# Performance work log

Measured on AMD Instinct MI355X. Metric: run time of the kernel, lower is better.

Reference implementation:

```python
import jax, jax.numpy as jnp
import numpy as np

F, OUT = 256, 16
H = [128, 128, 64]
B = 8192


def _normed(v, g):
    # weight_norm (torch default dim=0): w[o,:] = g[o] * v[o,:] / ||v[o,:]||
    # v: [F, out, in], g: [F, out]
    return g[..., None] * v / jnp.linalg.norm(v, axis=-1, keepdims=True)


def setup_inputs() -> dict:
    key = jax.random.key(0)
    ks = jax.random.split(key, 12)
    s = 0.1
    return {
        "tabular": jax.random.normal(ks[0], (B, 2, F), dtype=jnp.float32),
        # input layer: Linear(1, H[0]) per feature, stacked over F
        "v_in": jax.random.normal(ks[1], (F, H[0], 1), dtype=jnp.float32) * s,
        "g_in": jnp.ones((F, H[0]), dtype=jnp.float32),
        "b_in": jax.random.normal(ks[2], (F, H[0]), dtype=jnp.float32) * s,
        # dense_0: Linear(H[0], H[1])
        "v_h0": jax.random.normal(ks[3], (F, H[1], H[0]), dtype=jnp.float32) * s,
        "g_h0": jnp.ones((F, H[1]), dtype=jnp.float32),
        "b_h0": jax.random.normal(ks[4], (F, H[1]), dtype=jnp.float32) * s,
        # dense_1: Linear(H[1], H[2])
        "v_h1": jax.random.normal(ks[5], (F, H[2], H[1]), dtype=jnp.float32) * s,
        "g_h1": jnp.ones((F, H[2]), dtype=jnp.float32),
        "b_h1": jax.random.normal(ks[6], (F, H[2]), dtype=jnp.float32) * s,
        # dense_out: Linear(H[2], OUT, bias=False)
        "v_out": jax.random.normal(ks[7], (F, OUT, H[2]), dtype=jnp.float32) * s,
        "g_out": jnp.ones((F, OUT), dtype=jnp.float32),
        "bias": jnp.zeros((1, OUT), dtype=jnp.float32),
    }


def reference(tabular, v_in, g_in, b_in, v_h0, g_h0, b_h0, v_h1, g_h1, b_h1,
              v_out, g_out, bias):
    values, is_missing = tabular[:, 0, :], tabular[:, 1, :]  # [B, F]
    x = values * (1.0 - is_missing)
    # input layer: in-dim is 1, so it's an outer product with the weight column
    w0 = _normed(v_in, g_in)[:, :, 0]                       # [F, H0]
    h = jax.nn.relu(x[:, :, None] * w0[None] + b_in[None])  # [B, F, H0]
    # hidden layers (dropout is identity in eval mode)
    h = jax.nn.relu(jnp.einsum("bfi,foi->bfo", h, _normed(v_h0, g_h0)) + b_h0[None])
    h = jax.nn.relu(jnp.einsum("bfi,foi->bfo", h, _normed(v_h1, g_h1)) + b_h1[None])
    outputs = jnp.einsum("bfi,foi->bfo", h, _normed(v_out, g_out))  # [B, F, OUT]
    # feature_dropout is identity in eval mode
    logits = jnp.sum(outputs, axis=1) + bias                # [B, OUT]
    return logits, outputs
```

## Files before the change

### kernel.cpp

```cpp
#include <hip/hip_runtime.h>

typedef unsigned short u16;
typedef unsigned int   u32;
typedef __attribute__((ext_vector_type(8))) short bf16x8;
typedef __attribute__((ext_vector_type(4))) float f32x4;
typedef __attribute__((ext_vector_type(2))) float f32x2;

#define NFEAT  256
#define NBATCH 8192
#define BT     128
#define NBT    (NBATCH / BT)
#define ITERS  8

__device__ __forceinline__ u16 f2bf(float f) {
    u32 u = __builtin_bit_cast(u32, f);
    return (u16)((u + 0x7FFFu + ((u >> 16) & 1u)) >> 16);
}
__device__ __forceinline__ u32 cvtpk(float a, float b) {
    u32 r;
    asm("v_cvt_pk_bf16_f32 %0, %1, %2" : "=v"(r) : "v"(a), "v"(b));
    return r;
}
__device__ __forceinline__ f32x4 mfma16(bf16x8 a, bf16x8 b, f32x4 c) {
    return __builtin_amdgcn_mfma_f32_16x16x32_bf16(a, b, c, 0, 0, 0);
}
__device__ __forceinline__ bf16x8 frag_word0(u32 word0) {
    union { bf16x8 v; u32 w[4]; } u;
    u.w[0] = word0; u.w[1] = 0; u.w[2] = 0; u.w[3] = 0;
    return u.v;
}
__device__ __forceinline__ char* swz(char* base, int b, int col2) {
    return base + b * 256 + (col2 ^ ((b & 15) << 4));
}
__device__ __forceinline__ const char* swz(const char* base, int b, int col2) {
    return base + b * 256 + (col2 ^ ((b & 15) << 4));
}
__device__ __forceinline__ uint2 relu_pk4(f32x4 v, f32x4 bs) {
    f32x4 s = v + bs;
    return make_uint2(cvtpk(fmaxf(s[0], 0.f), fmaxf(s[1], 0.f)),
                      cvtpk(fmaxf(s[2], 0.f), fmaxf(s[3], 0.f)));
}
__device__ __forceinline__ void barrier_lgkm() {
    asm volatile("s_waitcnt lgkmcnt(0)" ::: "memory");
    __builtin_amdgcn_s_barrier();
    asm volatile("" ::: "memory");
}

__global__ void prep_w0(const float* __restrict__ v_in, const float* __restrict__ g_in,
                        u16* __restrict__ w0) {
    int i = blockIdx.x * blockDim.x + threadIdx.x;
    float v = v_in[i];
    float g = g_in[i];
    w0[i] = f2bf(v >= 0.f ? g : -g);
}

__global__ void prep_norm(const float* __restrict__ v_h0, const float* __restrict__ g_h0,
                          const float* __restrict__ v_h1, const float* __restrict__ g_h1,
                          const float* __restrict__ v_out, const float* __restrict__ g_out,
                          u16* __restrict__ w1, u16* __restrict__ w2, u16* __restrict__ w3) {
    const int wave = (blockIdx.x * blockDim.x + threadIdx.x) >> 6;
    const int lane = threadIdx.x & 63;
    if (wave < 32768 + 16384) {
        const float* src; u16* dst; float g;
        if (wave < 32768) {
            src = v_h0 + (size_t)wave * 128; dst = w1 + (size_t)wave * 128; g = g_h0[wave];
        } else {
            int r = wave - 32768;
            src = v_h1 + (size_t)r * 128; dst = w2 + (size_t)r * 128; g = g_h1[r];
        }
        f32x2 v = *(const f32x2*)(src + lane * 2);
        float ss = v[0] * v[0] + v[1] * v[1];
        #pragma unroll
        for (int off = 32; off; off >>= 1) ss += __shfl_xor(ss, off);
        float s = g * rsqrtf(ss);
        *(u32*)(dst + lane * 2) = cvtpk(v[0] * s, v[1] * s);
    } else {
        int r = wave - 49152;
        const float* src = v_out + (size_t)r * 64;
        float v = src[lane];
        float ss = v * v;
        #pragma unroll
        for (int off = 32; off; off >>= 1) ss += __shfl_xor(ss, off);
        float s = g_out[r] * rsqrtf(ss);
        w3[(size_t)r * 64 + lane] = f2bf(v * s);
    }
}

__global__ void prep_x(const float* __restrict__ tab, u16* __restrict__ x_t) {
    __shared__ u16 tile[64][65];
    const int bb = (blockIdx.x % (NBATCH / 64)) * 64;
    const int ff = (blockIdx.x / (NBATCH / 64)) * 64;
    const int tr = threadIdx.x >> 6;
    const int tc = threadIdx.x & 63;
    #pragma unroll
    for (int i = 0; i < 16; i++) {
        int b = bb + tr + i * 4;
        float val  = tab[(size_t)b * 512 + ff + tc];
        float miss = tab[(size_t)b * 512 + 256 + ff + tc];
        tile[tr + i * 4][tc] = f2bf(val * (1.f - miss));
    }
    __syncthreads();
    #pragma unroll
    for (int i = 0; i < 16; i++) {
        int fr = tr + i * 4;
        x_t[(size_t)(ff + fr) * NBATCH + bb + tc] = tile[tc][fr];
    }
}

__global__ void reduce_logits(const float* __restrict__ outputs,
                              const float* __restrict__ bias,
                              float* __restrict__ logits) {
    const int b = blockIdx.x * 4 + (threadIdx.x >> 6);
    const int lane = threadIdx.x & 63;
    const int j4 = lane & 3;
    const int fo = lane >> 2;
    const float* base = outputs + (size_t)b * (NFEAT * 16);
    f32x4 acc = {};
    #pragma unroll
    for (int it = 0; it < 16; it++) {
        f32x4 v = *(const f32x4*)(base + (fo + it * 16) * 16 + j4 * 4);
        acc[0] += v[0]; acc[1] += v[1]; acc[2] += v[2]; acc[3] += v[3];
    }
    #pragma unroll
    for (int off = 4; off < 64; off <<= 1) {
        acc[0] += __shfl_xor(acc[0], off);
        acc[1] += __shfl_xor(acc[1], off);
        acc[2] += __shfl_xor(acc[2], off);
        acc[3] += __shfl_xor(acc[3], off);
    }
    if (lane < 4) {
        f32x4 bs = *(const f32x4*)(bias + lane * 4);
        acc[0] += bs[0]; acc[1] += bs[1]; acc[2] += bs[2]; acc[3] += bs[3];
        *(f32x4*)(logits + b * 16 + lane * 4) = acc;
    }
}

__global__ __launch_bounds__(256, 2) void nam_main(
    const u16* __restrict__ x_t, const u16* __restrict__ w0g,
    const u16* __restrict__ w1g, const u16* __restrict__ w2g, const u16* __restrict__ w3g,
    const float* __restrict__ b_in, const float* __restrict__ b_h0, const float* __restrict__ b_h1,
    float* __restrict__ outputs)
{
    __shared__ u16 hA[BT * 128];
    __shared__ u16 hB[BT * 128];

    const int bid   = blockIdx.x;
    const int f     = (bid & 7) * 32 + ((bid >> 3) & 31);
    const int chunk = bid >> 8;
    const int t  = threadIdx.x;
    const int w  = t >> 6;
    const int wo = w >> 1;
    const int wb = w & 1;
    const int lane = t & 63;
    const int lo = lane & 15;
    const int hi = lane >> 4;

    bf16x8 a0f[4];
    #pragma unroll
    for (int m = 0; m < 4; m++) {
        const int o = f * 128 + wo * 64 + m * 16 + lo;
        float bi = b_in[o];
        u32 pk = (u32)w0g[o] | (cvtpk(bi, bi) << 16);
        a0f[m] = frag_word0(hi == 0 ? pk : 0u);
    }
    bf16x8 w1f[4][4];
    {
        const u16* base = w1g + ((size_t)(f * 128 + wo * 64 + lo)) * 128 + hi * 8;
        #pragma unroll
        for (int m = 0; m < 4; m++)
            #pragma unroll
            for (int ks = 0; ks < 4; ks++)
                w1f[m][ks] = *(const bf16x8*)(base + m * 2048 + ks * 32);
    }
    bf16x8 w2f[2][4];
    {
        const u16* base = w2g + ((size_t)(f * 64 + wo * 32 + lo)) * 128 + hi * 8;
        #pragma unroll
        for (int m = 0; m < 2; m++)
            #pragma unroll
            for (int ks = 0; ks < 4; ks++)
                w2f[m][ks] = *(const bf16x8*)(base + m * 2048 + ks * 32);
    }
    bf16x8 w3f[2];
    {
        const u16* base = w3g + ((size_t)(f * 16 + lo)) * 64 + hi * 8;
        #pragma unroll
        for (int ks = 0; ks < 2; ks++)
            w3f[ks] = *(const bf16x8*)(base + ks * 32);
    }
    f32x4 bs1[4];
    #pragma unroll
    for (int m = 0; m < 4; m++)
        bs1[m] = *(const f32x4*)(b_h0 + f * 128 + wo * 64 + m * 16 + hi * 4);
    f32x4 bs2[2];
    #pragma unroll
    for (int m = 0; m < 2; m++)
        bs2[m] = *(const f32x4*)(b_h1 + f * 64 + wo * 32 + m * 16 + hi * 4);

    const u16* xbase = x_t + (size_t)f * NBATCH;

    u32 xw[4];
    {
        const int bt0 = chunk * ITERS;
        #pragma unroll
        for (int n = 0; n < 4; n++)
            xw[n] = (u32)xbase[bt0 * BT + wb * 64 + n * 16 + lo];
    }

    for (int it = 0; it < ITERS; it++) {
        const int bt = chunk * ITERS + it;

        barrier_lgkm();

        {
            bf16x8 bm[4];
            #pragma unroll
            for (int n = 0; n < 4; n++)
                bm[n] = frag_word0(hi == 0 ? (xw[n] | 0x3F800000u) : 0u);
            #pragma unroll
            for (int m = 0; m < 4; m++) {
                #pragma unroll
                for (int n = 0; n < 4; n++) {
                    f32x4 d = mfma16(a0f[m], bm[n], f32x4{});
                    const int b = wb * 64 + n * 16 + lo;
                    const int col2 = (wo * 64 + m * 16 + hi * 4) * 2;
                    *(uint2*)swz((char*)hA, b, col2) =
                        make_uint2(cvtpk(fmaxf(0.f, d[0]), fmaxf(0.f, d[1])),
                                   cvtpk(fmaxf(0.f, d[2]), fmaxf(0.f, d[3])));
                }
            }
        }
        barrier_lgkm();

        {
            if (it + 1 < ITERS) {
                #pragma unroll
                for (int n = 0; n < 4; n++)
                    xw[n] = (u32)xbase[(bt + 1) * BT + wb * 64 + n * 16 + lo];
            }
            f32x4 acc[4][4] = {};
            #pragma unroll
            for (int ks = 0; ks < 4; ks++) {
                bf16x8 bm[4];
                #pragma unroll
                for (int n = 0; n < 4; n++) {
                    const int b = wb * 64 + n * 16 + lo;
                    bm[n] = *(const bf16x8*)swz((const char*)hA, b, ks * 64 + hi * 16);
                }
                __builtin_amdgcn_s_setprio(1);
                #pragma unroll
                for (int m = 0; m < 4; m++)
                    #pragma unroll
                    for (int n = 0; n < 4; n++)
                        acc[m][n] = mfma16(w1f[m][ks], bm[n], acc[m][n]);
                __builtin_amdgcn_s_setprio(0);
            }
            #pragma unroll
            for (int m = 0; m < 4; m++) {
                const int col2 = (wo * 64 + m * 16 + hi * 4) * 2;
                #pragma unroll
                for (int n = 0; n < 4; n++) {
                    const int b = wb * 64 + n * 16 + lo;
                    *(uint2*)swz((char*)hB, b, col2) = relu_pk4(acc[m][n], bs1[m]);
                }
            }
        }
        barrier_lgkm();

        {
            f32x4 acc[2][4] = {};
            #pragma unroll
            for (int ks = 0; ks < 4; ks++) {
                bf16x8 bm[4];
                #pragma unroll
                for (int n = 0; n < 4; n++) {
                    const int b = wb * 64 + n * 16 + lo;
                    bm[n] = *(const bf16x8*)swz((const char*)hB, b, ks * 64 + hi * 16);
                }
                __builtin_amdgcn_s_setprio(1);
                #pragma unroll
                for (int m = 0; m < 2; m++)
                    #pragma unroll
                    for (int n = 0; n < 4; n++)
                        acc[m][n] = mfma16(w2f[m][ks], bm[n], acc[m][n]);
                __builtin_amdgcn_s_setprio(0);
            }
            #pragma unroll
            for (int m = 0; m < 2; m++) {
                const int col2 = (wo * 32 + m * 16 + hi * 4) * 2;
                #pragma unroll
                for (int n = 0; n < 4; n++) {
                    const int b = wb * 64 + n * 16 + lo;
                    *(uint2*)swz((char*)hA, b, col2) = relu_pk4(acc[m][n], bs2[m]);
                }
            }
        }
        barrier_lgkm();

        {
            f32x4 acc[2] = {};
            #pragma unroll
            for (int ks = 0; ks < 2; ks++) {
                #pragma unroll
                for (int n = 0; n < 2; n++) {
                    const int b = w * 32 + n * 16 + lo;
                    bf16x8 bm = *(const bf16x8*)swz((const char*)hA, b, ks * 64 + hi * 16);
                    acc[n] = mfma16(w3f[ks], bm, acc[n]);
                }
            }
            #pragma unroll
            for (int n = 0; n < 2; n++) {
                const int gb = bt * BT + w * 32 + n * 16 + lo;
                float* op = outputs + ((size_t)gb * NFEAT + f) * 16 + hi * 4;
                *(f32x4*)op = acc[n];
            }
        }
    }
}

extern "C" void kernel_launch(void* const* d_in, const int* in_sizes, int n_in,
                              void* d_out, int out_size, void* d_ws, size_t ws_size,
                              hipStream_t stream) {
    const float* tab   = (const float*)d_in[0];
    const float* v_in  = (const float*)d_in[1];
    const float* g_in  = (const float*)d_in[2];
    const float* b_in  = (const float*)d_in[3];
    const float* v_h0  = (const float*)d_in[4];
    const float* g_h0  = (const float*)d_in[5];
    const float* b_h0  = (const float*)d_in[6];
    const float* v_h1  = (const float*)d_in[7];
    const float* g_h1  = (const float*)d_in[8];
    const float* b_h1  = (const float*)d_in[9];
    const float* v_out = (const float*)d_in[10];
    const float* g_out = (const float*)d_in[11];
    const float* bias  = (const float*)d_in[12];

    char* ws = (char*)d_ws;
    u16* w0  = (u16*)(ws);
    u16* w1  = (u16*)(ws + 65536);
    u16* w2  = (u16*)(ws + 65536 + 8388608);
    u16* w3  = (u16*)(ws + 12648448);
    u16* x_t = (u16*)(ws + 13172736);

    float* logits  = (float*)d_out;
    float* outputs = (float*)d_out + (size_t)NBATCH * 16;

    hipLaunchKernelGGL(prep_w0,   dim3(128),   dim3(256), 0, stream, v_in, g_in, w0);
    hipLaunchKernelGGL(prep_norm, dim3(13312), dim3(256), 0, stream,
                       v_h0, g_h0, v_h1, g_h1, v_out, g_out, w1, w2, w3);
    hipLaunchKernelGGL(prep_x,    dim3(512),   dim3(256), 0, stream, tab, x_t);
    hipLaunchKernelGGL(nam_main,  dim3(NFEAT * NBT / ITERS), dim3(256), 0, stream,
                       x_t, w0, w1, w2, w3, b_in, b_h0, b_h1, outputs);
    hipLaunchKernelGGL(reduce_logits, dim3(NBATCH / 4), dim3(256), 0, stream,
                       outputs, bias, logits);
}
```

Baseline: 181.8 us.

## Split nam_main work across 8 waves per block to cut per-wave registers

Result: slower. 265.7 us (+46.1%).

```diff
diff --git a/kernel.cpp b/kernel.cpp
--- a/kernel.cpp
+++ b/kernel.cpp
@@ -135,7 +135,7 @@
     }
 }
 
-__global__ __launch_bounds__(256, 2) void nam_main(
+__global__ __launch_bounds__(512, 4) void nam_main(
     const u16* __restrict__ x_t, const u16* __restrict__ w0g,
     const u16* __restrict__ w1g, const u16* __restrict__ w2g, const u16* __restrict__ w3g,
     const float* __restrict__ b_in, const float* __restrict__ b_h0, const float* __restrict__ b_h1,
@@ -149,37 +149,34 @@
     const int chunk = bid >> 8;
     const int t  = threadIdx.x;
     const int w  = t >> 6;
-    const int wo = w >> 1;
-    const int wb = w & 1;
+    const int wq = w & 3;
+    const int wh = w >> 2;
     const int lane = t & 63;
     const int lo = lane & 15;
     const int hi = lane >> 4;
 
-    bf16x8 a0f[4];
-    #pragma unroll
-    for (int m = 0; m < 4; m++) {
-        const int o = f * 128 + wo * 64 + m * 16 + lo;
+    u32 a0pk[2];
+    #pragma unroll
+    for (int m = 0; m < 2; m++) {
+        const int o = f * 128 + wq * 32 + m * 16 + lo;
         float bi = b_in[o];
-        u32 pk = (u32)w0g[o] | (cvtpk(bi, bi) << 16);
-        a0f[m] = frag_word0(hi == 0 ? pk : 0u);
-    }
-    bf16x8 w1f[4][4];
+        a0pk[m] = (u32)w0g[o] | (cvtpk(bi, bi) << 16);
+    }
+    bf16x8 w1f[2][4];
     {
-        const u16* base = w1g + ((size_t)(f * 128 + wo * 64 + lo)) * 128 + hi * 8;
-        #pragma unroll
-        for (int m = 0; m < 4; m++)
+        const u16* base = w1g + ((size_t)(f * 128 + wq * 32 + lo)) * 128 + hi * 8;
+        #pragma unroll
+        for (int m = 0; m < 2; m++)
             #pragma unroll
             for (int ks = 0; ks < 4; ks++)
                 w1f[m][ks] = *(const bf16x8*)(base + m * 2048 + ks * 32);
     }
-    bf16x8 w2f[2][4];
+    bf16x8 w2f[4];
     {
-        const u16* base = w2g + ((size_t)(f * 64 + wo * 32 + lo)) * 128 + hi * 8;
-        #pragma unroll
-        for (int m = 0; m < 2; m++)
-            #pragma unroll
-            for (int ks = 0; ks < 4; ks++)
-                w2f[m][ks] = *(const bf16x8*)(base + m * 2048 + ks * 32);
+        const u16* base = w2g + ((size_t)(f * 64 + wq * 16 + lo)) * 128 + hi * 8;
+        #pragma unroll
+        for (int ks = 0; ks < 4; ks++)
+            w2f[ks] = *(const bf16x8*)(base + ks * 32);
     }
     bf16x8 w3f[2];
     {
@@ -188,14 +185,11 @@
         for (int ks = 0; ks < 2; ks++)
             w3f[ks] = *(const bf16x8*)(base + ks * 32);
     }
-    f32x4 bs1[4];
-    #pragma unroll
-    for (int m = 0; m < 4; m++)
-        bs1[m] = *(const f32x4*)(b_h0 + f * 128 + wo * 64 + m * 16 + hi * 4);
-    f32x4 bs2[2];
+    f32x4 bs1[2];
     #pragma unroll
     for (int m = 0; m < 2; m++)
-        bs2[m] = *(const f32x4*)(b_h1 + f * 64 + wo * 32 + m * 16 + hi * 4);
+        bs1[m] = *(const f32x4*)(b_h0 + f * 128 + wq * 32 + m * 16 + hi * 4);
+    f32x4 bs2 = *(const f32x4*)(b_h1 + f * 64 + wq * 16 + hi * 4);
 
     const u16* xbase = x_t + (size_t)f * NBATCH;
 
@@ -204,7 +198,7 @@
         const int bt0 = chunk * ITERS;
         #pragma unroll
         for (int n = 0; n < 4; n++)
-            xw[n] = (u32)xbase[bt0 * BT + wb * 64 + n * 16 + lo];
+            xw[n] = (u32)xbase[bt0 * BT + wh * 64 + n * 16 + lo];
     }
 
     for (int it = 0; it < ITERS; it++) {
@@ -218,12 +212,13 @@
             for (int n = 0; n < 4; n++)
                 bm[n] = frag_word0(hi == 0 ? (xw[n] | 0x3F800000u) : 0u);
             #pragma unroll
-            for (int m = 0; m < 4; m++) {
+            for (int m = 0; m < 2; m++) {
+                bf16x8 a0 = frag_word0(hi == 0 ? a0pk[m] : 0u);
                 #pragma unroll
                 for (int n = 0; n < 4; n++) {
-                    f32x4 d = mfma16(a0f[m], bm[n], f32x4{});
-                    const int b = wb * 64 + n * 16 + lo;
-                    const int col2 = (wo * 64 + m * 16 + hi * 4) * 2;
+                    f32x4 d = mfma16(a0, bm[n], f32x4{});
+                    const int b = wh * 64 + n * 16 + lo;
+                    const int col2 = (wq * 32 + m * 16 + hi * 4) * 2;
                     *(uint2*)swz((char*)hA, b, col2) =
                         make_uint2(cvtpk(fmaxf(0.f, d[0]), fmaxf(0.f, d[1])),
                                    cvtpk(fmaxf(0.f, d[2]), fmaxf(0.f, d[3])));
@@ -236,31 +231,31 @@
             if (it + 1 < ITERS) {
                 #pragma unroll
                 for (int n = 0; n < 4; n++)
-                    xw[n] = (u32)xbase[(bt + 1) * BT + wb * 64 + n * 16 + lo];
-            }
-            f32x4 acc[4][4] = {};
+                    xw[n] = (u32)xbase[(bt + 1) * BT + wh * 64 + n * 16 + lo];
+            }
+            f32x4 acc[2][4] = {};
             #pragma unroll
             for (int ks = 0; ks < 4; ks++) {
                 bf16x8 bm[4];
                 #pragma unroll
                 for (int n = 0; n < 4; n++) {
-                    const int b = wb * 64 + n * 16 + lo;
+                    const int b = wh * 64 + n * 16 + lo;
                     bm[n] = *(const bf16x8*)swz((const char*)hA, b, ks * 64 + hi * 16);
                 }
                 __builtin_amdgcn_s_setprio(1);
                 #pragma unroll
-                for (int m = 0; m < 4; m++)
+                for (int m = 0; m < 2; m++)
                     #pragma unroll
                     for (int n = 0; n < 4; n++)
                         acc[m][n] = mfma16(w1f[m][ks], bm[n], acc[m][n]);
                 __builtin_amdgcn_s_setprio(0);
             }
             #pragma unroll
-            for (int m = 0; m < 4; m++) {
-                const int col2 = (wo * 64 + m * 16 + hi * 4) * 2;
+            for (int m = 0; m < 2; m++) {
+                const int col2 = (wq * 32 + m * 16 + hi * 4) * 2;
                 #pragma unroll
                 for (int n = 0; n < 4; n++) {
-                    const int b = wb * 64 + n * 16 + lo;
+                    const int b = wh * 64 + n * 16 + lo;
                     *(uint2*)swz((char*)hB, b, col2) = relu_pk4(acc[m][n], bs1[m]);
                 }
             }
@@ -268,52 +263,41 @@
         barrier_lgkm();
 
         {
-            f32x4 acc[2][4] = {};
+            f32x4 acc[4] = {};
             #pragma unroll
             for (int ks = 0; ks < 4; ks++) {
                 bf16x8 bm[4];
                 #pragma unroll
                 for (int n = 0; n < 4; n++) {
-                    const int b = wb * 64 + n * 16 + lo;
+                    const int b = wh * 64 + n * 16 + lo;
                     bm[n] = *(const bf16x8*)swz((const char*)hB, b, ks * 64 + hi * 16);
                 }
                 __builtin_amdgcn_s_setprio(1);
                 #pragma unroll
-                for (int m = 0; m < 2; m++)
-                    #pragma unroll
-                    for (int n = 0; n < 4; n++)
-                        acc[m][n] = mfma16(w2f[m][ks], bm[n], acc[m][n]);
+                for (int n = 0; n < 4; n++)
+                    acc[n] = mfma16(w2f[ks], bm[n], acc[n]);
                 __builtin_amdgcn_s_setprio(0);
             }
-            #pragma unroll
-            for (int m = 0; m < 2; m++) {
-                const int col2 = (wo * 32 + m * 16 + hi * 4) * 2;
-                #pragma unroll
-                for (int n = 0; n < 4; n++) {
-                    const int b = wb * 64 + n * 16 + lo;
-                    *(uint2*)swz((char*)hA, b, col2) = relu_pk4(acc[m][n], bs2[m]);
-                }
+            const int col2 = (wq * 16 + hi * 4) * 2;
+            #pragma unroll
+            for (int n = 0; n < 4; n++) {
+                const int b = wh * 64 + n * 16 + lo;
+                *(uint2*)swz((char*)hA, b, col2) = relu_pk4(acc[n], bs2);
             }
         }
         barrier_lgkm();
 
         {
-            f32x4 acc[2] = {};
+            f32x4 acc = {};
+            const int b = w * 16 + lo;
             #pragma unroll
             for (int ks = 0; ks < 2; ks++) {
-                #pragma unroll
-                for (int n = 0; n < 2; n++) {
-                    const int b = w * 32 + n * 16 + lo;
-                    bf16x8 bm = *(const bf16x8*)swz((const char*)hA, b, ks * 64 + hi * 16);
-                    acc[n] = mfma16(w3f[ks], bm, acc[n]);
-                }
-            }
-            #pragma unroll
-            for (int n = 0; n < 2; n++) {
-                const int gb = bt * BT + w * 32 + n * 16 + lo;
-                float* op = outputs + ((size_t)gb * NFEAT + f) * 16 + hi * 4;
-                *(f32x4*)op = acc[n];
-            }
+                bf16x8 bm = *(const bf16x8*)swz((const char*)hA, b, ks * 64 + hi * 16);
+                acc = mfma16(w3f[ks], bm, acc);
+            }
+            const int gb = bt * BT + b;
+            float* op = outputs + ((size_t)gb * NFEAT + f) * 16 + hi * 4;
+            *(f32x4*)op = acc;
         }
     }
 }
@@ -349,7 +333,7 @@
     hipLaunchKernelGGL(prep_norm, dim3(13312), dim3(256), 0, stream,
                        v_h0, g_h0, v_h1, g_h1, v_out, g_out, w1, w2, w3);
     hipLaunchKernelGGL(prep_x,    dim3(512),   dim3(256), 0, stream, tab, x_t);
-    hipLaunchKernelGGL(nam_main,  dim3(NFEAT * NBT / ITERS), dim3(256), 0, stream,
+    hipLaunchKernelGGL(nam_main,  dim3(NFEAT * NBT / ITERS), dim3(512), 0, stream,
                        x_t, w0, w1, w2, w3, b_in, b_h0, b_h1, outputs);
     hipLaunchKernelGGL(reduce_logits, dim3(NBATCH / 4), dim3(256), 0, stream,
                        outputs, bias, logits);
```
